# Kernel optimization log

Hardware: AMD Instinct MI355X
Metric: run time of the kernel (lower is better)

Reference implementation:

```python
import jax, jax.numpy as jnp
import numpy as np

N, E, G = 10000, 160000, 64          # nodes, edges, graphs in batch
X_IN, HID, EDIM, H = 128, 128, 32, 4  # feature dims, edge dim, heads
NEG_SLOPE = 0.2


def setup_inputs() -> dict:
    key = jax.random.key(0)
    ks = jax.random.split(key, 24)
    def p(k, shape):
        return jax.random.normal(k, shape, jnp.float32) * 0.1
    inp = {
        "x": jax.random.normal(ks[0], (N, X_IN), jnp.float32),
        "edge_index": jax.random.randint(ks[1], (2, E), 0, N),
        "edge_attr": jax.random.normal(ks[2], (E, EDIM), jnp.float32),
        "batch": jnp.sort(jax.random.randint(ks[3], (N,), 0, G)),
    }
    dims = [(X_IN, HID), (HID, 2 * HID), (2 * HID, HID)]
    i = 4
    for l, (cin, cout) in enumerate(dims, 1):
        inp[f"W{l}"] = p(ks[i], (cin, H * cout)); i += 1   # node lin (bias-free, PyG default)
        inp[f"We{l}"] = p(ks[i], (EDIM, H * cout)); i += 1  # edge lin (bias=False in PyG)
        inp[f"as{l}"] = p(ks[i], (H, cout)); i += 1         # att_src
        inp[f"ad{l}"] = p(ks[i], (H, cout)); i += 1         # att_dst
        inp[f"ae{l}"] = p(ks[i], (H, cout)); i += 1         # att_edge
        inp[f"b{l}"] = jnp.zeros((cout,), jnp.float32); i += 1
    return inp


def _add_self_loops(src, dst, eattr, n):
    # PyG GATConv default: add_self_loops=True, fill_value='mean' ->
    # self-loop edge_attr = scatter-mean of incoming edge_attr per node.
    deg = jax.ops.segment_sum(jnp.ones_like(dst, jnp.float32), dst, num_segments=n)
    mean_e = jax.ops.segment_sum(eattr, dst, num_segments=n) / jnp.maximum(deg, 1.0)[:, None]
    loop = jnp.arange(n)
    return (jnp.concatenate([src, loop]), jnp.concatenate([dst, loop]),
            jnp.concatenate([eattr, mean_e], axis=0))


def _segment_softmax(logits, seg, n):
    # logits: [E2, H], softmax over edges grouped by destination node
    m = jax.ops.segment_max(logits, seg, num_segments=n)
    m = jnp.where(jnp.isfinite(m), m, 0.0)
    ex = jnp.exp(logits - m[seg])
    s = jax.ops.segment_sum(ex, seg, num_segments=n)
    return ex / (s[seg] + 1e-16)


def _gat_layer(x, src, dst, eattr, W, We, a_s, a_d, a_e, b, n):
    heads, cout = a_s.shape
    xs = (x @ W).reshape(n, heads, cout)            # [N,H,C]
    ee = (eattr @ We).reshape(-1, heads, cout)      # [E2,H,C]
    al_src = jnp.sum(xs * a_s, axis=-1)             # [N,H]
    al_dst = jnp.sum(xs * a_d, axis=-1)             # [N,H]
    al_edge = jnp.sum(ee * a_e, axis=-1)            # [E2,H]
    logits = jax.nn.leaky_relu(al_src[src] + al_dst[dst] + al_edge, NEG_SLOPE)
    alpha = _segment_softmax(logits, dst, n)        # [E2,H]
    out = jax.ops.segment_sum(alpha[:, :, None] * xs[src], dst, num_segments=n)
    return out.mean(axis=1) + b                     # concat=False -> mean over heads


def reference(x, edge_index, edge_attr, batch,
              W1, We1, as1, ad1, ae1, b1,
              W2, We2, as2, ad2, ae2, b2,
              W3, We3, as3, ad3, ae3, b3):
    src, dst = edge_index[0], edge_index[1]
    src2, dst2, e2 = _add_self_loops(src, dst, edge_attr, N)
    h = jax.nn.elu(_gat_layer(x, src2, dst2, e2, W1, We1, as1, ad1, ae1, b1, N))
    h = jax.nn.elu(_gat_layer(h, src2, dst2, e2, W2, We2, as2, ad2, ae2, b2, N))
    h = jax.nn.elu(_gat_layer(h, src2, dst2, e2, W3, We3, as3, ad3, ae3, b3, N))
    cnt = jax.ops.segment_sum(jnp.ones((N,), jnp.float32), batch, num_segments=G)
    return jax.ops.segment_sum(h, batch, num_segments=G) / jnp.maximum(cnt, 1.0)[:, None]
```

## Files before the change

kernel.cpp:

```cpp
#include <hip/hip_runtime.h>

#define NN 10000
#define NE 160000
#define NE2 (NE + NN)
#define NG 64
#define EDIM 32

typedef _Float16 f16;
typedef __attribute__((ext_vector_type(2))) _Float16 f16x2;
typedef __attribute__((ext_vector_type(4))) _Float16 f16x4;
typedef __attribute__((ext_vector_type(8))) _Float16 f16x8;
typedef __attribute__((ext_vector_type(4))) float f32x4;
typedef __attribute__((ext_vector_type(8))) unsigned short u16x8;

__device__ __forceinline__ float lrelu(float x) { return fmaxf(x, 0.2f * x); }
__device__ __forceinline__ float elu1(float x) { return x > 0.f ? x : __expf(x) - 1.f; }


__global__ __launch_bounds__(256) void k_prep(const int* __restrict__ ei,
                                              int* __restrict__ deg,
                                              const float* __restrict__ x,
                                              f16* __restrict__ x16) {
    int b = blockIdx.x, tid = threadIdx.x;
    if (b < 625) {
        int e = b * 256 + tid;
        atomicAdd(&deg[ei[NE + e]], 1);
    } else {
        int i = (b - 625) * 256 + tid;
        float4 v = ((const float4*)x)[i];
        f16x4 o;
        o[0] = (f16)v.x; o[1] = (f16)v.y; o[2] = (f16)v.z; o[3] = (f16)v.w;
        *(f16x4*)(x16 + i * 4) = o;
    }
}


__global__ __launch_bounds__(1024) void k_scan2(const int* __restrict__ deg,
                                                int* __restrict__ row_ptr,
                                                int* __restrict__ cursor,
                                                const int* __restrict__ batch,
                                                float* __restrict__ invc) {
    int tid = threadIdx.x;
    int vals[10];
    int run = 0;
#pragma unroll
    for (int i = 0; i < 10; ++i) {
        int n = tid * 10 + i;
        int v = (n < NN) ? (deg[n] + 1) : 0;
        run += v;
        vals[i] = run;
    }
    int total = run;
    int lane = tid & 63, wid = tid >> 6;
    int sc = total;
#pragma unroll
    for (int off = 1; off < 64; off <<= 1) {
        int t = __shfl_up(sc, off);
        if (lane >= off) sc += t;
    }
    __shared__ int wsum[16];
    if (lane == 63) wsum[wid] = sc;
    __syncthreads();
    if (tid == 0) {
        int a = 0;
#pragma unroll
        for (int w = 0; w < 16; ++w) { int t = wsum[w]; wsum[w] = a; a += t; }
    }
    __syncthreads();
    int excl = sc - total + wsum[wid];
#pragma unroll
    for (int i = 0; i < 10; ++i) {
        int n = tid * 10 + i;
        if (n < NN) {
            int prev = i ? vals[i - 1] : 0;
            row_ptr[n + 1] = excl + vals[i];
            cursor[n] = excl + prev;
        }
    }
    if (tid == 0) row_ptr[0] = 0;
    if (tid < NG) {
        int g = tid;
        int lo = 0, hi = NN;
        while (lo < hi) { int mid = (lo + hi) >> 1; if (batch[mid] < g) lo = mid + 1; else hi = mid; }
        int start = lo;
        lo = start; hi = NN;
        while (lo < hi) { int mid = (lo + hi) >> 1; if (batch[mid] < g + 1) lo = mid + 1; else hi = mid; }
        invc[g] = 1.f / fmaxf((float)(lo - start), 1.f);
    }
}

__global__ void k_fill(const int* __restrict__ ei, int* __restrict__ cursor,
                       int* __restrict__ src_sorted, int* __restrict__ eid_sorted,
                       int* __restrict__ pos) {
    int e = blockIdx.x * blockDim.x + threadIdx.x;
    if (e >= NE2) return;
    int s, d;
    if (e < NE) { s = ei[e]; d = ei[NE + e]; }
    else        { s = d = e - NE; }
    int p = atomicAdd(&cursor[d], 1);
    src_sorted[p] = s;
    eid_sorted[p] = e;
    pos[e] = p;
}

__global__ __launch_bounds__(256) void k_esum(const int* __restrict__ row_ptr,
                                              const int* __restrict__ eid_sorted,
                                              const float* __restrict__ eattr,
                                              float* __restrict__ esum) {
    int wid = threadIdx.x >> 6, lane = threadIdx.x & 63;
    int node = blockIdx.x * 4 + wid;
    int d = lane & 31, sel = lane >> 5;
    int beg = row_ptr[node], end = row_ptr[node + 1];
    float v = 0.f;
    for (int j = beg + sel; j < end; j += 2) {
        int eid = eid_sorted[j];
        if (eid < NE) v += eattr[(size_t)eid * EDIM + d];
    }
    v += __shfl_xor(v, 32);
    if (sel == 0) esum[node * EDIM + d] = v;
}


template <int CIN, int C>
__device__ __forceinline__ void wprep_body(int b, int tid,
                                           const float* __restrict__ W,
                                           const float* __restrict__ We,
                                           const float* __restrict__ as_,
                                           const float* __restrict__ ad_,
                                           const float* __restrict__ ae_,
                                           f16* __restrict__ Bt,
                                           float* __restrict__ asd,
                                           float* __restrict__ Wf,
                                           float (*t)[33]) {
    constexpr int K4 = 4 * CIN;
    constexpr int KT = CIN / 32, CT = C / 32;
    constexpr int TB = 4 * KT * CT;
    constexpr int FB = CIN / 64;
    if (b < TB) {
        int h = b / (KT * CT);
        int rem = b % (KT * CT);
        int k0 = (rem / CT) * 32, c0 = (rem % CT) * 32;
        int i = tid >> 5, j = tid & 31;
#pragma unroll
        for (int it = 0; it < 4; ++it)
            t[i + it * 8][j] = W[(size_t)(k0 + i + it * 8) * (4 * C) + h * C + c0 + j];
        __syncthreads();
#pragma unroll
        for (int it = 0; it < 4; ++it) {
            int jj = (tid >> 5) + it * 8, ii = tid & 31;
            Bt[(size_t)(c0 + jj) * K4 + h * CIN + k0 + ii] = (f16)t[ii][jj];
        }
    } else if (b < TB + FB) {
        int k = (b - TB) * 64 + (tid >> 2), h = tid & 3;
        const float4* wr = (const float4*)(W + (size_t)k * (4 * C) + h * C);
        const float4* a4 = (const float4*)(as_ + h * C);
        const float4* d4 = (const float4*)(ad_ + h * C);
        float s = 0.f, d = 0.f;
        for (int c = 0; c < C / 4; ++c) {
            float4 w = wr[c], av = a4[c], dv = d4[c];
            s += w.x * av.x + w.y * av.y + w.z * av.z + w.w * av.w;
            d += w.x * dv.x + w.y * dv.y + w.z * dv.z + w.w * dv.w;
        }
        asd[h * CIN + k] = s;
        asd[4 * CIN + h * CIN + k] = d;
    } else if (tid < 128) {
        int dd = tid >> 2, h = tid & 3;
        const float4* wr = (const float4*)(We + (size_t)dd * (4 * C) + h * C);
        const float4* a4 = (const float4*)(ae_ + h * C);
        float s = 0.f;
        for (int c = 0; c < C / 4; ++c) {
            float4 w = wr[c], av = a4[c];
            s += w.x * av.x + w.y * av.y + w.z * av.z + w.w * av.w;
        }
        Wf[dd * 4 + h] = s;
    }
}

__global__ __launch_bounds__(256) void k_wprep_all(
    const float* W1, const float* We1, const float* as1, const float* ad1, const float* ae1,
    f16* Bt1, float* asd1, float* Wf1,
    const float* W2, const float* We2, const float* as2, const float* ad2, const float* ae2,
    f16* Bt2, float* asd2, float* Wf2,
    const float* W3, const float* We3, const float* as3, const float* ad3, const float* ae3,
    f16* Bt3, float* asd3, float* Wf3) {
    __shared__ float t[32][33];
    int b = blockIdx.x, tid = threadIdx.x;
    if (b < 67)       wprep_body<128, 128>(b,       tid, W1, We1, as1, ad1, ae1, Bt1, asd1, Wf1, t);
    else if (b < 198) wprep_body<128, 256>(b - 67,  tid, W2, We2, as2, ad2, ae2, Bt2, asd2, Wf2, t);
    else              wprep_body<256, 128>(b - 198, tid, W3, We3, as3, ad3, ae3, Bt3, asd3, Wf3, t);
}

__global__ __launch_bounds__(256) void k_e4(const float* __restrict__ eattr,
                                            const float* __restrict__ esum,
                                            const int* __restrict__ deg,
                                            const float* __restrict__ Wf1,
                                            const float* __restrict__ Wf2,
                                            const float* __restrict__ Wf3,
                                            const int* __restrict__ pos,
                                            float* __restrict__ e4all) {
    __shared__ float wf[3][128];
    int tid = threadIdx.x;
    if (tid < 128) { wf[0][tid] = Wf1[tid]; wf[1][tid] = Wf2[tid]; wf[2][tid] = Wf3[tid]; }
    __syncthreads();
    int e = blockIdx.x * 256 + tid;
    if (e >= NE2) return;
    const float4* er;
    float scale = 1.f;
    if (e < NE) {
        er = (const float4*)(eattr + (size_t)e * EDIM);
    } else {
        int n = e - NE;
        er = (const float4*)(esum + (size_t)n * EDIM);
        scale = 1.f / fmaxf((float)deg[n], 1.f);
    }
    float4 v[8];
#pragma unroll
    for (int i = 0; i < 8; ++i) v[i] = er[i];
    int p = pos[e];
#pragma unroll
    for (int l = 0; l < 3; ++l) {
        float a0 = 0.f, a1 = 0.f, a2 = 0.f, a3 = 0.f;
#pragma unroll
        for (int d4 = 0; d4 < 8; ++d4) {
            const float* w = &wf[l][d4 * 16];
            a0 += v[d4].x * w[0] + v[d4].y * w[4] + v[d4].z * w[8]  + v[d4].w * w[12];
            a1 += v[d4].x * w[1] + v[d4].y * w[5] + v[d4].z * w[9]  + v[d4].w * w[13];
            a2 += v[d4].x * w[2] + v[d4].y * w[6] + v[d4].z * w[10] + v[d4].w * w[14];
            a3 += v[d4].x * w[3] + v[d4].y * w[7] + v[d4].z * w[11] + v[d4].w * w[15];
        }
        ((float4*)e4all)[(size_t)l * NE2 + p] =
            make_float4(a0 * scale, a1 * scale, a2 * scale, a3 * scale);
    }
}

template <int CIN>
__global__ __launch_bounds__(256) void k_alnode2(const f16* __restrict__ xp,
                                                 const float* __restrict__ asd,
                                                 float* __restrict__ als,
                                                 float* __restrict__ ald) {
    __shared__ float sA[4 * CIN], sD[4 * CIN];
    for (int i = threadIdx.x; i < 4 * CIN; i += 256) { sA[i] = asd[i]; sD[i] = asd[4 * CIN + i]; }
    __syncthreads();
    int wid = threadIdx.x >> 6, lane = threadIdx.x & 63;
    int node = blockIdx.x * 4 + wid;
    int h = lane >> 4, c16 = lane & 15;
    constexpr int KC = CIN / 16;
    const f16* xr = xp + (size_t)node * CIN + c16 * KC;
    float s = 0.f, d = 0.f;
#pragma unroll
    for (int p = 0; p < KC / 8; ++p) {
        f16x8 v = *(const f16x8*)(xr + p * 8);
        const float* wa = &sA[h * CIN + c16 * KC + p * 8];
        const float* wd = &sD[h * CIN + c16 * KC + p * 8];
#pragma unroll
        for (int i = 0; i < 8; ++i) {
            float f = (float)v[i];
            s += f * wa[i];
            d += f * wd[i];
        }
    }
#pragma unroll
    for (int off = 1; off < 16; off <<= 1) { s += __shfl_xor(s, off); d += __shfl_xor(d, off); }
    if (c16 == 0) { als[node * 4 + h] = s; ald[node * 4 + h] = d; }
}

template <int CIN>
__global__ __launch_bounds__(256) void k_agg2(const int* __restrict__ row_ptr,
                                              const int* __restrict__ src_sorted,
                                              const float* __restrict__ e4,
                                              const float* __restrict__ als,
                                              const float* __restrict__ ald,
                                              const f16* __restrict__ xp,
                                              f16* __restrict__ aggcat) {
    constexpr int EPL = CIN / 64;
    int wid = threadIdx.x >> 6, lane = threadIdx.x & 63;
    int node = blockIdx.x * 4 + wid;
    int beg = row_ptr[node], end = row_ptr[node + 1];
    float4 ad4 = ((const float4*)ald)[node];
    const float4* e44 = (const float4*)e4;
    const float4* als4 = (const float4*)als;
    float s0 = 0.f, s1 = 0.f, s2 = 0.f, s3 = 0.f;
    float a0[EPL] = {}, a1[EPL] = {}, a2[EPL] = {}, a3[EPL] = {};
    const f16* xbase = xp + lane * EPL;
#pragma unroll 4
    for (int j = beg; j < end; ++j) {
        int src = src_sorted[j];
        float4 ev = e44[j];
        float4 av = als4[src];
        float e0 = __expf(lrelu(ev.x + av.x + ad4.x));
        float e1 = __expf(lrelu(ev.y + av.y + ad4.y));
        float e2 = __expf(lrelu(ev.z + av.z + ad4.z));
        float e3 = __expf(lrelu(ev.w + av.w + ad4.w));
        s0 += e0; s1 += e1; s2 += e2; s3 += e3;
        const f16* xr = xbase + (size_t)src * CIN;
        if (EPL == 2) {
            f16x2 v = *(const f16x2*)xr;
            float f0 = (float)v[0], f1 = (float)v[1];
            a0[0] += e0 * f0; a0[1] += e0 * f1;
            a1[0] += e1 * f0; a1[1] += e1 * f1;
            a2[0] += e2 * f0; a2[1] += e2 * f1;
            a3[0] += e3 * f0; a3[1] += e3 * f1;
        } else {
            f16x4 v = *(const f16x4*)xr;
#pragma unroll
            for (int i = 0; i < 4; ++i) {
                float f = (float)v[i];
                a0[i] += e0 * f; a1[i] += e1 * f; a2[i] += e2 * f; a3[i] += e3 * f;
            }
        }
    }
    float i0 = 1.f / (s0 + 1e-16f), i1 = 1.f / (s1 + 1e-16f);
    float i2 = 1.f / (s2 + 1e-16f), i3 = 1.f / (s3 + 1e-16f);
    f16* ob = aggcat + (size_t)node * 4 * CIN + lane * EPL;
    if (EPL == 2) {
        f16x2 o;
        o[0] = (f16)(a0[0] * i0); o[1] = (f16)(a0[1] * i0); *(f16x2*)(ob + 0 * CIN) = o;
        o[0] = (f16)(a1[0] * i1); o[1] = (f16)(a1[1] * i1); *(f16x2*)(ob + 1 * CIN) = o;
        o[0] = (f16)(a2[0] * i2); o[1] = (f16)(a2[1] * i2); *(f16x2*)(ob + 2 * CIN) = o;
        o[0] = (f16)(a3[0] * i3); o[1] = (f16)(a3[1] * i3); *(f16x2*)(ob + 3 * CIN) = o;
    } else {
        f16x4 o;
#pragma unroll
        for (int i = 0; i < 4; ++i) o[i] = (f16)(a0[i] * i0);
        *(f16x4*)(ob + 0 * CIN) = o;
#pragma unroll
        for (int i = 0; i < 4; ++i) o[i] = (f16)(a1[i] * i1);
        *(f16x4*)(ob + 1 * CIN) = o;
#pragma unroll
        for (int i = 0; i < 4; ++i) o[i] = (f16)(a2[i] * i2);
        *(f16x4*)(ob + 2 * CIN) = o;
#pragma unroll
        for (int i = 0; i < 4; ++i) o[i] = (f16)(a3[i] * i3);
        *(f16x4*)(ob + 3 * CIN) = o;
    }
}

template <int K4, int C>
__global__ __launch_bounds__(256) void k_gemm_ep(const f16* __restrict__ A,
                                                 const f16* __restrict__ Bt,
                                                 const float* __restrict__ bias,
                                                 f16* __restrict__ hout) {
    __shared__ f16 Als[64 * 40];
    __shared__ f16 Bls[64 * 40];
    int bm = blockIdx.x * 64, bn = blockIdx.y * 64;
    int tid = threadIdx.x;
    int wid = tid >> 6, lane = tid & 63;
    int wrow = (wid >> 1) * 32, wcol = (wid & 1) * 32;
    int fr = lane & 15, fk = (lane >> 4) * 8;
    f32x4 acc[2][2];
#pragma unroll
    for (int m = 0; m < 2; ++m)
#pragma unroll
        for (int n = 0; n < 2; ++n) acc[m][n] = (f32x4){0.f, 0.f, 0.f, 0.f};

    int srow = tid >> 2, spart = tid & 3;
    for (int k0 = 0; k0 < K4; k0 += 32) {
        int gr = bm + srow;
        u16x8 va = (u16x8)0;
        if (gr < NN) va = *(const u16x8*)(A + (size_t)gr * K4 + k0 + spart * 8);
        *(u16x8*)&Als[srow * 40 + spart * 8] = va;
        u16x8 vb = *(const u16x8*)(Bt + (size_t)(bn + srow) * K4 + k0 + spart * 8);
        *(u16x8*)&Bls[srow * 40 + spart * 8] = vb;
        __syncthreads();
        f16x8 af[2], bf[2];
        af[0] = *(const f16x8*)&Als[(wrow + fr) * 40 + fk];
        af[1] = *(const f16x8*)&Als[(wrow + 16 + fr) * 40 + fk];
        bf[0] = *(const f16x8*)&Bls[(wcol + fr) * 40 + fk];
        bf[1] = *(const f16x8*)&Bls[(wcol + 16 + fr) * 40 + fk];
#pragma unroll
        for (int m = 0; m < 2; ++m)
#pragma unroll
            for (int n = 0; n < 2; ++n)
                acc[m][n] = __builtin_amdgcn_mfma_f32_16x16x32_f16(af[m], bf[n], acc[m][n], 0, 0, 0);
        __syncthreads();
    }

    int cr = (lane >> 4) * 4, cc = lane & 15;
    float b0 = bias[bn + wcol + cc], b1 = bias[bn + wcol + 16 + cc];
#pragma unroll
    for (int m = 0; m < 2; ++m) {
#pragma unroll
        for (int r = 0; r < 4; ++r) {
            int row = bm + wrow + m * 16 + cr + r;
            if (row >= NN) continue;
            f16* cp = hout + (size_t)row * C + bn + wcol + cc;
            cp[0]  = (f16)elu1(0.25f * acc[m][0][r] + b0);
            cp[16] = (f16)elu1(0.25f * acc[m][1][r] + b1);
        }
    }
}

template <int K4, int C>
__global__ __launch_bounds__(256) void k_gemm_pool(const f16* __restrict__ A,
                                                   const f16* __restrict__ Bt,
                                                   const float* __restrict__ bias,
                                                   const int* __restrict__ batch,
                                                   const float* __restrict__ invc,
                                                   float* __restrict__ out) {
    __shared__ f16 Als[64 * 40];
    __shared__ f16 Bls[64 * 40];
    int bm = blockIdx.x * 64, bn = blockIdx.y * 64;
    int tid = threadIdx.x;
    int wid = tid >> 6, lane = tid & 63;
    int wrow = (wid >> 1) * 32, wcol = (wid & 1) * 32;
    int fr = lane & 15, fk = (lane >> 4) * 8;
    f32x4 acc[2][2];
#pragma unroll
    for (int m = 0; m < 2; ++m)
#pragma unroll
        for (int n = 0; n < 2; ++n) acc[m][n] = (f32x4){0.f, 0.f, 0.f, 0.f};

    int srow = tid >> 2, spart = tid & 3;
    for (int k0 = 0; k0 < K4; k0 += 32) {
        int gr = bm + srow;
        u16x8 va = (u16x8)0;
        if (gr < NN) va = *(const u16x8*)(A + (size_t)gr * K4 + k0 + spart * 8);
        *(u16x8*)&Als[srow * 40 + spart * 8] = va;
        u16x8 vb = *(const u16x8*)(Bt + (size_t)(bn + srow) * K4 + k0 + spart * 8);
        *(u16x8*)&Bls[srow * 40 + spart * 8] = vb;
        __syncthreads();
        f16x8 af[2], bf[2];
        af[0] = *(const f16x8*)&Als[(wrow + fr) * 40 + fk];
        af[1] = *(const f16x8*)&Als[(wrow + 16 + fr) * 40 + fk];
        bf[0] = *(const f16x8*)&Bls[(wcol + fr) * 40 + fk];
        bf[1] = *(const f16x8*)&Bls[(wcol + 16 + fr) * 40 + fk];
#pragma unroll
        for (int m = 0; m < 2; ++m)
#pragma unroll
            for (int n = 0; n < 2; ++n)
                acc[m][n] = __builtin_amdgcn_mfma_f32_16x16x32_f16(af[m], bf[n], acc[m][n], 0, 0, 0);
        __syncthreads();
    }

    int cr = (lane >> 4) * 4, cc = lane & 15;
    float b0 = bias[bn + wcol + cc], b1 = bias[bn + wcol + 16 + cc];
#pragma unroll
    for (int m = 0; m < 2; ++m) {
#pragma unroll
        for (int r = 0; r < 4; ++r) {
            int row = bm + wrow + m * 16 + cr + r;
            if (row >= NN) continue;
            int g = batch[row];
            float ic = invc[g];
            float* op = out + (size_t)g * C + bn + wcol + cc;
            atomicAdd(op,      elu1(0.25f * acc[m][0][r] + b0) * ic);
            atomicAdd(op + 16, elu1(0.25f * acc[m][1][r] + b1) * ic);
        }
    }
}


struct Ws {
    f16 *x16, *hA, *hB, *aggcat, *Wt1, *Wt2, *Wt3;
    float *als, *ald, *esum, *e4all, *asd1, *asd2, *asd3, *Wf1, *Wf2, *Wf3, *invc;
    int *deg, *row_ptr, *cursor, *src_sorted, *eid_sorted, *pos;
};

static void carve(void* base, Ws& w) {
    char* p = (char*)base;
    size_t off = 0;
    auto take = [&](size_t bytes) {
        off = (off + 255) & ~(size_t)255;
        void* r = p + off;
        off += bytes;
        return r;
    };
    w.x16        = (f16*)take((size_t)NN * 128 * 2);
    w.hA         = (f16*)take((size_t)NN * 128 * 2);
    w.hB         = (f16*)take((size_t)NN * 256 * 2);
    w.aggcat     = (f16*)take((size_t)NN * 1024 * 2);
    w.Wt1        = (f16*)take((size_t)512 * 128 * 2);
    w.Wt2        = (f16*)take((size_t)512 * 256 * 2);
    w.Wt3        = (f16*)take((size_t)1024 * 128 * 2);
    w.als        = (float*)take((size_t)NN * 4 * 4);
    w.ald        = (float*)take((size_t)NN * 4 * 4);
    w.esum       = (float*)take((size_t)NN * EDIM * 4);
    w.e4all      = (float*)take((size_t)3 * NE2 * 4 * 4);
    w.asd1       = (float*)take(2 * 4 * 128 * 4);
    w.asd2       = (float*)take(2 * 4 * 128 * 4);
    w.asd3       = (float*)take(2 * 4 * 256 * 4);
    w.Wf1        = (float*)take(128 * 4);
    w.Wf2        = (float*)take(128 * 4);
    w.Wf3        = (float*)take(128 * 4);
    w.invc       = (float*)take(NG * 4);
    w.deg        = (int*)take((size_t)NN * 4);
    w.row_ptr    = (int*)take((size_t)(NN + 1) * 4);
    w.cursor     = (int*)take((size_t)NN * 4);
    w.src_sorted = (int*)take((size_t)NE2 * 4);
    w.eid_sorted = (int*)take((size_t)NE2 * 4);
    w.pos        = (int*)take((size_t)NE2 * 4);
}

extern "C" void kernel_launch(void* const* d_in, const int* in_sizes, int n_in,
                              void* d_out, int out_size, void* d_ws, size_t ws_size,
                              hipStream_t stream) {
    const float* x     = (const float*)d_in[0];
    const int*   ei    = (const int*)d_in[1];
    const float* eattr = (const float*)d_in[2];
    const int*   batch = (const int*)d_in[3];
    const float* W[3]  = {(const float*)d_in[4],  (const float*)d_in[10], (const float*)d_in[16]};
    const float* We[3] = {(const float*)d_in[5],  (const float*)d_in[11], (const float*)d_in[17]};
    const float* as_[3]= {(const float*)d_in[6],  (const float*)d_in[12], (const float*)d_in[18]};
    const float* ad_[3]= {(const float*)d_in[7],  (const float*)d_in[13], (const float*)d_in[19]};
    const float* ae_[3]= {(const float*)d_in[8],  (const float*)d_in[14], (const float*)d_in[20]};
    const float* b_[3] = {(const float*)d_in[9],  (const float*)d_in[15], (const float*)d_in[21]};
    float* out = (float*)d_out;

    Ws w;
    carve(d_ws, w);

    hipMemsetAsync(w.deg, 0, (size_t)NN * 4, stream);
    hipMemsetAsync(out, 0, (size_t)NG * 128 * 4, stream);

    k_wprep_all<<<331, 256, 0, stream>>>(
        W[0], We[0], as_[0], ad_[0], ae_[0], w.Wt1, w.asd1, w.Wf1,
        W[1], We[1], as_[1], ad_[1], ae_[1], w.Wt2, w.asd2, w.Wf2,
        W[2], We[2], as_[2], ad_[2], ae_[2], w.Wt3, w.asd3, w.Wf3);

    k_prep<<<1875, 256, 0, stream>>>(ei, w.deg, x, w.x16);
    k_scan2<<<1, 1024, 0, stream>>>(w.deg, w.row_ptr, w.cursor, batch, w.invc);
    k_fill<<<(NE2 + 255) / 256, 256, 0, stream>>>(ei, w.cursor, w.src_sorted,
                                                  w.eid_sorted, w.pos);
    k_esum<<<NN / 4, 256, 0, stream>>>(w.row_ptr, w.eid_sorted, eattr, w.esum);
    k_e4<<<(NE2 + 255) / 256, 256, 0, stream>>>(eattr, w.esum, w.deg,
                                                w.Wf1, w.Wf2, w.Wf3, w.pos, w.e4all);

    const float* e4_1 = w.e4all;
    const float* e4_2 = w.e4all + (size_t)NE2 * 4;
    const float* e4_3 = w.e4all + (size_t)2 * NE2 * 4;

    k_alnode2<128><<<NN / 4, 256, 0, stream>>>(w.x16, w.asd1, w.als, w.ald);
    k_agg2<128><<<NN / 4, 256, 0, stream>>>(w.row_ptr, w.src_sorted, e4_1, w.als, w.ald,
                                            w.x16, w.aggcat);
    k_gemm_ep<512, 128><<<dim3(157, 2), 256, 0, stream>>>(w.aggcat, w.Wt1, b_[0], w.hA);

    k_alnode2<128><<<NN / 4, 256, 0, stream>>>(w.hA, w.asd2, w.als, w.ald);
    k_agg2<128><<<NN / 4, 256, 0, stream>>>(w.row_ptr, w.src_sorted, e4_2, w.als, w.ald,
                                            w.hA, w.aggcat);
    k_gemm_ep<512, 256><<<dim3(157, 4), 256, 0, stream>>>(w.aggcat, w.Wt2, b_[1], w.hB);

    k_alnode2<256><<<NN / 4, 256, 0, stream>>>(w.hB, w.asd3, w.als, w.ald);
    k_agg2<256><<<NN / 4, 256, 0, stream>>>(w.row_ptr, w.src_sorted, e4_3, w.als, w.ald,
                                            w.hB, w.aggcat);
    k_gemm_pool<1024, 128><<<dim3(157, 2), 256, 0, stream>>>(w.aggcat, w.Wt3, b_[2],
                                                             batch, w.invc, out);
}
```

Before: 348.7 us.

## Fuse preprocessing kernels, compute self-loop edge logits from projected values, fold alnode into GEMM epilogue

Merges weight prep, degree counting, x-to-f16 conversion and graph counts into one init kernel, and fuses the CSR fill with edge-logit projection and layer-1 node attention. Self-loop edge logits are now the mean of the already-projected incoming edge logits (linearity), which removes the esum pass, eid_sorted and pos. The layer 2/3 node attention scalars are computed in the previous GEMM epilogue via shuffles and atomics, which removes the separate alnode kernels. The aim is fewer launches and less memory traffic, at the cost of extra atomics and a nondeterministic float summation order.

```diff
diff --git a/kernel.cpp b/kernel.cpp
--- a/kernel.cpp
+++ b/kernel.cpp
@@ -15,110 +15,6 @@
 
 __device__ __forceinline__ float lrelu(float x) { return fmaxf(x, 0.2f * x); }
 __device__ __forceinline__ float elu1(float x) { return x > 0.f ? x : __expf(x) - 1.f; }
-
-
-__global__ __launch_bounds__(256) void k_prep(const int* __restrict__ ei,
-                                              int* __restrict__ deg,
-                                              const float* __restrict__ x,
-                                              f16* __restrict__ x16) {
-    int b = blockIdx.x, tid = threadIdx.x;
-    if (b < 625) {
-        int e = b * 256 + tid;
-        atomicAdd(&deg[ei[NE + e]], 1);
-    } else {
-        int i = (b - 625) * 256 + tid;
-        float4 v = ((const float4*)x)[i];
-        f16x4 o;
-        o[0] = (f16)v.x; o[1] = (f16)v.y; o[2] = (f16)v.z; o[3] = (f16)v.w;
-        *(f16x4*)(x16 + i * 4) = o;
-    }
-}
-
-
-__global__ __launch_bounds__(1024) void k_scan2(const int* __restrict__ deg,
-                                                int* __restrict__ row_ptr,
-                                                int* __restrict__ cursor,
-                                                const int* __restrict__ batch,
-                                                float* __restrict__ invc) {
-    int tid = threadIdx.x;
-    int vals[10];
-    int run = 0;
-#pragma unroll
-    for (int i = 0; i < 10; ++i) {
-        int n = tid * 10 + i;
-        int v = (n < NN) ? (deg[n] + 1) : 0;
-        run += v;
-        vals[i] = run;
-    }
-    int total = run;
-    int lane = tid & 63, wid = tid >> 6;
-    int sc = total;
-#pragma unroll
-    for (int off = 1; off < 64; off <<= 1) {
-        int t = __shfl_up(sc, off);
-        if (lane >= off) sc += t;
-    }
-    __shared__ int wsum[16];
-    if (lane == 63) wsum[wid] = sc;
-    __syncthreads();
-    if (tid == 0) {
-        int a = 0;
-#pragma unroll
-        for (int w = 0; w < 16; ++w) { int t = wsum[w]; wsum[w] = a; a += t; }
-    }
-    __syncthreads();
-    int excl = sc - total + wsum[wid];
-#pragma unroll
-    for (int i = 0; i < 10; ++i) {
-        int n = tid * 10 + i;
-        if (n < NN) {
-            int prev = i ? vals[i - 1] : 0;
-            row_ptr[n + 1] = excl + vals[i];
-            cursor[n] = excl + prev;
-        }
-    }
-    if (tid == 0) row_ptr[0] = 0;
-    if (tid < NG) {
-        int g = tid;
-        int lo = 0, hi = NN;
-        while (lo < hi) { int mid = (lo + hi) >> 1; if (batch[mid] < g) lo = mid + 1; else hi = mid; }
-        int start = lo;
-        lo = start; hi = NN;
-        while (lo < hi) { int mid = (lo + hi) >> 1; if (batch[mid] < g + 1) lo = mid + 1; else hi = mid; }
-        invc[g] = 1.f / fmaxf((float)(lo - start), 1.f);
-    }
-}
-
-__global__ void k_fill(const int* __restrict__ ei, int* __restrict__ cursor,
-                       int* __restrict__ src_sorted, int* __restrict__ eid_sorted,
-                       int* __restrict__ pos) {
-    int e = blockIdx.x * blockDim.x + threadIdx.x;
-    if (e >= NE2) return;
-    int s, d;
-    if (e < NE) { s = ei[e]; d = ei[NE + e]; }
-    else        { s = d = e - NE; }
-    int p = atomicAdd(&cursor[d], 1);
-    src_sorted[p] = s;
-    eid_sorted[p] = e;
-    pos[e] = p;
-}
-
-__global__ __launch_bounds__(256) void k_esum(const int* __restrict__ row_ptr,
-                                              const int* __restrict__ eid_sorted,
-                                              const float* __restrict__ eattr,
-                                              float* __restrict__ esum) {
-    int wid = threadIdx.x >> 6, lane = threadIdx.x & 63;
-    int node = blockIdx.x * 4 + wid;
-    int d = lane & 31, sel = lane >> 5;
-    int beg = row_ptr[node], end = row_ptr[node + 1];
-    float v = 0.f;
-    for (int j = beg + sel; j < end; j += 2) {
-        int eid = eid_sorted[j];
-        if (eid < NE) v += eattr[(size_t)eid * EDIM + d];
-    }
-    v += __shfl_xor(v, 32);
-    if (sel == 0) esum[node * EDIM + d] = v;
-}
 
 
 template <int CIN, int C>
@@ -176,93 +72,178 @@
     }
 }
 
-__global__ __launch_bounds__(256) void k_wprep_all(
+
+__global__ __launch_bounds__(256) void k_init(
     const float* W1, const float* We1, const float* as1, const float* ad1, const float* ae1,
     f16* Bt1, float* asd1, float* Wf1,
     const float* W2, const float* We2, const float* as2, const float* ad2, const float* ae2,
     f16* Bt2, float* asd2, float* Wf2,
     const float* W3, const float* We3, const float* as3, const float* ad3, const float* ae3,
-    f16* Bt3, float* asd3, float* Wf3) {
+    f16* Bt3, float* asd3, float* Wf3,
+    const int* ei, int* deg, const float* x, f16* x16,
+    const int* batch, float* invc) {
     __shared__ float t[32][33];
     int b = blockIdx.x, tid = threadIdx.x;
-    if (b < 67)       wprep_body<128, 128>(b,       tid, W1, We1, as1, ad1, ae1, Bt1, asd1, Wf1, t);
-    else if (b < 198) wprep_body<128, 256>(b - 67,  tid, W2, We2, as2, ad2, ae2, Bt2, asd2, Wf2, t);
-    else              wprep_body<256, 128>(b - 198, tid, W3, We3, as3, ad3, ae3, Bt3, asd3, Wf3, t);
-}
-
-__global__ __launch_bounds__(256) void k_e4(const float* __restrict__ eattr,
-                                            const float* __restrict__ esum,
-                                            const int* __restrict__ deg,
-                                            const float* __restrict__ Wf1,
-                                            const float* __restrict__ Wf2,
-                                            const float* __restrict__ Wf3,
-                                            const int* __restrict__ pos,
-                                            float* __restrict__ e4all) {
-    __shared__ float wf[3][128];
+    if (b < 67) {
+        wprep_body<128, 128>(b, tid, W1, We1, as1, ad1, ae1, Bt1, asd1, Wf1, t);
+    } else if (b < 198) {
+        wprep_body<128, 256>(b - 67, tid, W2, We2, as2, ad2, ae2, Bt2, asd2, Wf2, t);
+    } else if (b < 331) {
+        wprep_body<256, 128>(b - 198, tid, W3, We3, as3, ad3, ae3, Bt3, asd3, Wf3, t);
+    } else if (b < 956) {
+        int e = (b - 331) * 256 + tid;
+        atomicAdd(&deg[ei[NE + e]], 1);
+    } else if (b < 2206) {
+        int i = (b - 956) * 256 + tid;
+        float4 v = ((const float4*)x)[i];
+        f16x4 o;
+        o[0] = (f16)v.x; o[1] = (f16)v.y; o[2] = (f16)v.z; o[3] = (f16)v.w;
+        *(f16x4*)(x16 + i * 4) = o;
+    } else if (tid < NG) {
+        int g = tid;
+        int lo = 0, hi = NN;
+        while (lo < hi) { int mid = (lo + hi) >> 1; if (batch[mid] < g) lo = mid + 1; else hi = mid; }
+        int start = lo;
+        lo = start; hi = NN;
+        while (lo < hi) { int mid = (lo + hi) >> 1; if (batch[mid] < g + 1) lo = mid + 1; else hi = mid; }
+        invc[g] = 1.f / fmaxf((float)(lo - start), 1.f);
+    }
+}
+
+
+__global__ __launch_bounds__(1024) void k_scan2(const int* __restrict__ deg,
+                                                int* __restrict__ row_ptr,
+                                                int* __restrict__ cursor) {
     int tid = threadIdx.x;
-    if (tid < 128) { wf[0][tid] = Wf1[tid]; wf[1][tid] = Wf2[tid]; wf[2][tid] = Wf3[tid]; }
+    int vals[10];
+    int run = 0;
+#pragma unroll
+    for (int i = 0; i < 10; ++i) {
+        int n = tid * 10 + i;
+        int v = (n < NN) ? (deg[n] + 1) : 0;
+        run += v;
+        vals[i] = run;
+    }
+    int total = run;
+    int lane = tid & 63, wid = tid >> 6;
+    int sc = total;
+#pragma unroll
+    for (int off = 1; off < 64; off <<= 1) {
+        int t = __shfl_up(sc, off);
+        if (lane >= off) sc += t;
+    }
+    __shared__ int wsum[16];
+    if (lane == 63) wsum[wid] = sc;
     __syncthreads();
-    int e = blockIdx.x * 256 + tid;
-    if (e >= NE2) return;
-    const float4* er;
-    float scale = 1.f;
-    if (e < NE) {
-        er = (const float4*)(eattr + (size_t)e * EDIM);
+    if (tid == 0) {
+        int a = 0;
+#pragma unroll
+        for (int w = 0; w < 16; ++w) { int t = wsum[w]; wsum[w] = a; a += t; }
+    }
+    __syncthreads();
+    int excl = sc - total + wsum[wid];
+#pragma unroll
+    for (int i = 0; i < 10; ++i) {
+        int n = tid * 10 + i;
+        if (n < NN) {
+            int prev = i ? vals[i - 1] : 0;
+            row_ptr[n + 1] = excl + vals[i];
+            cursor[n] = excl + prev;
+        }
+    }
+    if (tid == 0) row_ptr[0] = 0;
+}
+
+
+__global__ __launch_bounds__(256) void k_fill_e4(const int* __restrict__ ei,
+                                                 int* __restrict__ cursor,
+                                                 int* __restrict__ src_sorted,
+                                                 int* __restrict__ selfpos,
+                                                 const float* __restrict__ eattr,
+                                                 const float* __restrict__ Wf1,
+                                                 const float* __restrict__ Wf2,
+                                                 const float* __restrict__ Wf3,
+                                                 float* __restrict__ e4all,
+                                                 const f16* __restrict__ x16,
+                                                 const float* __restrict__ asd1,
+                                                 float* __restrict__ als1,
+                                                 float* __restrict__ ald1) {
+    __shared__ float smem[1024];
+    int b = blockIdx.x, tid = threadIdx.x;
+    if (b < 665) {
+        for (int i = tid; i < 384; i += 256)
+            smem[i] = (i < 128) ? Wf1[i] : (i < 256) ? Wf2[i - 128] : Wf3[i - 256];
+        __syncthreads();
+        int e = b * 256 + tid;
+        if (e >= NE2) return;
+        if (e < NE) {
+            int s = ei[e], d = ei[NE + e];
+            int p = atomicAdd(&cursor[d], 1);
+            src_sorted[p] = s;
+            float4 v[8];
+            const float4* er = (const float4*)(eattr + (size_t)e * EDIM);
+#pragma unroll
+            for (int i = 0; i < 8; ++i) v[i] = er[i];
+#pragma unroll
+            for (int l = 0; l < 3; ++l) {
+                float a0 = 0.f, a1 = 0.f, a2 = 0.f, a3 = 0.f;
+#pragma unroll
+                for (int d4 = 0; d4 < 8; ++d4) {
+                    const float* w = &smem[l * 128 + d4 * 16];
+                    a0 += v[d4].x * w[0] + v[d4].y * w[4] + v[d4].z * w[8]  + v[d4].w * w[12];
+                    a1 += v[d4].x * w[1] + v[d4].y * w[5] + v[d4].z * w[9]  + v[d4].w * w[13];
+                    a2 += v[d4].x * w[2] + v[d4].y * w[6] + v[d4].z * w[10] + v[d4].w * w[14];
+                    a3 += v[d4].x * w[3] + v[d4].y * w[7] + v[d4].z * w[11] + v[d4].w * w[15];
+                }
+                ((float4*)e4all)[(size_t)l * NE2 + p] = make_float4(a0, a1, a2, a3);
+            }
+        } else {
+            int n = e - NE;
+            int p = atomicAdd(&cursor[n], 1);
+            src_sorted[p] = n;
+            selfpos[n] = p;
+        }
     } else {
-        int n = e - NE;
-        er = (const float4*)(esum + (size_t)n * EDIM);
-        scale = 1.f / fmaxf((float)deg[n], 1.f);
-    }
-    float4 v[8];
-#pragma unroll
-    for (int i = 0; i < 8; ++i) v[i] = er[i];
-    int p = pos[e];
-#pragma unroll
-    for (int l = 0; l < 3; ++l) {
-        float a0 = 0.f, a1 = 0.f, a2 = 0.f, a3 = 0.f;
-#pragma unroll
-        for (int d4 = 0; d4 < 8; ++d4) {
-            const float* w = &wf[l][d4 * 16];
-            a0 += v[d4].x * w[0] + v[d4].y * w[4] + v[d4].z * w[8]  + v[d4].w * w[12];
-            a1 += v[d4].x * w[1] + v[d4].y * w[5] + v[d4].z * w[9]  + v[d4].w * w[13];
-            a2 += v[d4].x * w[2] + v[d4].y * w[6] + v[d4].z * w[10] + v[d4].w * w[14];
-            a3 += v[d4].x * w[3] + v[d4].y * w[7] + v[d4].z * w[11] + v[d4].w * w[15];
-        }
-        ((float4*)e4all)[(size_t)l * NE2 + p] =
-            make_float4(a0 * scale, a1 * scale, a2 * scale, a3 * scale);
-    }
-}
-
-template <int CIN>
-__global__ __launch_bounds__(256) void k_alnode2(const f16* __restrict__ xp,
-                                                 const float* __restrict__ asd,
-                                                 float* __restrict__ als,
-                                                 float* __restrict__ ald) {
-    __shared__ float sA[4 * CIN], sD[4 * CIN];
-    for (int i = threadIdx.x; i < 4 * CIN; i += 256) { sA[i] = asd[i]; sD[i] = asd[4 * CIN + i]; }
-    __syncthreads();
-    int wid = threadIdx.x >> 6, lane = threadIdx.x & 63;
-    int node = blockIdx.x * 4 + wid;
-    int h = lane >> 4, c16 = lane & 15;
-    constexpr int KC = CIN / 16;
-    const f16* xr = xp + (size_t)node * CIN + c16 * KC;
-    float s = 0.f, d = 0.f;
-#pragma unroll
-    for (int p = 0; p < KC / 8; ++p) {
-        f16x8 v = *(const f16x8*)(xr + p * 8);
-        const float* wa = &sA[h * CIN + c16 * KC + p * 8];
-        const float* wd = &sD[h * CIN + c16 * KC + p * 8];
+        float* sA = smem;
+        float* sD = smem + 512;
+        for (int i = tid; i < 512; i += 256) { sA[i] = asd1[i]; sD[i] = asd1[512 + i]; }
+        __syncthreads();
+        int wid = tid >> 6, lane = tid & 63;
+        int node = (b - 665) * 4 + wid;
+        int h = lane >> 4, c16 = lane & 15;
+        const f16* xr = x16 + (size_t)node * 128 + c16 * 8;
+        f16x8 v = *(const f16x8*)xr;
+        float s = 0.f, d = 0.f;
 #pragma unroll
         for (int i = 0; i < 8; ++i) {
             float f = (float)v[i];
-            s += f * wa[i];
-            d += f * wd[i];
-        }
-    }
-#pragma unroll
-    for (int off = 1; off < 16; off <<= 1) { s += __shfl_xor(s, off); d += __shfl_xor(d, off); }
-    if (c16 == 0) { als[node * 4 + h] = s; ald[node * 4 + h] = d; }
-}
+            s += f * sA[h * 128 + c16 * 8 + i];
+            d += f * sD[h * 128 + c16 * 8 + i];
+        }
+#pragma unroll
+        for (int off = 1; off < 16; off <<= 1) { s += __shfl_xor(s, off); d += __shfl_xor(d, off); }
+        if (c16 == 0) { als1[node * 4 + h] = s; ald1[node * 4 + h] = d; }
+    }
+}
+
+
+__global__ __launch_bounds__(256) void k_e4self(const int* __restrict__ row_ptr,
+                                                const int* __restrict__ selfpos,
+                                                float* __restrict__ e4all) {
+    int t = blockIdx.x * 256 + threadIdx.x;
+    int node = t >> 4, sub = t & 15;
+    if (sub >= 12) return;
+    int l = sub >> 2, c = sub & 3;
+    int beg = row_ptr[node], end = row_ptr[node + 1];
+    int sp = selfpos[node];
+    const float* base = e4all + (size_t)l * NE2 * 4 + c;
+    float s = 0.f;
+    for (int j = beg; j < end; ++j)
+        if (j != sp) s += base[(size_t)j * 4];
+    float inv = 1.f / fmaxf((float)(end - beg - 1), 1.f);
+    e4all[(size_t)l * NE2 * 4 + (size_t)sp * 4 + c] = s * inv;
+}
+
 
 template <int CIN>
 __global__ __launch_bounds__(256) void k_agg2(const int* __restrict__ row_ptr,
@@ -335,11 +316,15 @@
     }
 }
 
-template <int K4, int C>
+
+template <int K4, int C, bool FUSE>
 __global__ __launch_bounds__(256) void k_gemm_ep(const f16* __restrict__ A,
                                                  const f16* __restrict__ Bt,
                                                  const float* __restrict__ bias,
-                                                 f16* __restrict__ hout) {
+                                                 f16* __restrict__ hout,
+                                                 const float* __restrict__ asd_n,
+                                                 float* __restrict__ als_n,
+                                                 float* __restrict__ ald_n) {
     __shared__ f16 Als[64 * 40];
     __shared__ f16 Bls[64 * 40];
     int bm = blockIdx.x * 64, bn = blockIdx.y * 64;
@@ -376,19 +361,56 @@
     }
 
     int cr = (lane >> 4) * 4, cc = lane & 15;
-    float b0 = bias[bn + wcol + cc], b1 = bias[bn + wcol + 16 + cc];
+    int col0 = bn + wcol + cc, col1 = col0 + 16;
+    float b0 = bias[col0], b1 = bias[col1];
+    float wa0[4], wa1[4], wd0[4], wd1[4];
+    if (FUSE) {
+#pragma unroll
+        for (int h = 0; h < 4; ++h) {
+            wa0[h] = asd_n[h * C + col0];
+            wa1[h] = asd_n[h * C + col1];
+            wd0[h] = asd_n[4 * C + h * C + col0];
+            wd1[h] = asd_n[4 * C + h * C + col1];
+        }
+    }
 #pragma unroll
     for (int m = 0; m < 2; ++m) {
 #pragma unroll
         for (int r = 0; r < 4; ++r) {
             int row = bm + wrow + m * 16 + cr + r;
             if (row >= NN) continue;
-            f16* cp = hout + (size_t)row * C + bn + wcol + cc;
-            cp[0]  = (f16)elu1(0.25f * acc[m][0][r] + b0);
-            cp[16] = (f16)elu1(0.25f * acc[m][1][r] + b1);
-        }
-    }
-}
+            float v0 = elu1(0.25f * acc[m][0][r] + b0);
+            float v1 = elu1(0.25f * acc[m][1][r] + b1);
+            f16* cp = hout + (size_t)row * C + col0;
+            cp[0]  = (f16)v0;
+            cp[16] = (f16)v1;
+            if (FUSE) {
+                float s[4], d[4];
+#pragma unroll
+                for (int h = 0; h < 4; ++h) {
+                    s[h] = v0 * wa0[h] + v1 * wa1[h];
+                    d[h] = v0 * wd0[h] + v1 * wd1[h];
+                }
+#pragma unroll
+                for (int off = 1; off < 16; off <<= 1) {
+#pragma unroll
+                    for (int h = 0; h < 4; ++h) {
+                        s[h] += __shfl_xor(s[h], off);
+                        d[h] += __shfl_xor(d[h], off);
+                    }
+                }
+                if (cc == 0) {
+#pragma unroll
+                    for (int h = 0; h < 4; ++h) {
+                        atomicAdd(&als_n[row * 4 + h], s[h]);
+                        atomicAdd(&ald_n[row * 4 + h], d[h]);
+                    }
+                }
+            }
+        }
+    }
+}
+
 
 template <int K4, int C>
 __global__ __launch_bounds__(256) void k_gemm_pool(const f16* __restrict__ A,
@@ -452,8 +474,11 @@
 
 struct Ws {
     f16 *x16, *hA, *hB, *aggcat, *Wt1, *Wt2, *Wt3;
-    float *als, *ald, *esum, *e4all, *asd1, *asd2, *asd3, *Wf1, *Wf2, *Wf3, *invc;
-    int *deg, *row_ptr, *cursor, *src_sorted, *eid_sorted, *pos;
+    float *als1, *ald1;
+    int *deg;
+    float *als2, *ald2, *als3, *ald3;
+    float *e4all, *asd1, *asd2, *asd3, *Wf1, *Wf2, *Wf3, *invc;
+    int *row_ptr, *cursor, *src_sorted, *selfpos;
 };
 
 static void carve(void* base, Ws& w) {
@@ -472,9 +497,13 @@
     w.Wt1        = (f16*)take((size_t)512 * 128 * 2);
     w.Wt2        = (f16*)take((size_t)512 * 256 * 2);
     w.Wt3        = (f16*)take((size_t)1024 * 128 * 2);
-    w.als        = (float*)take((size_t)NN * 4 * 4);
-    w.ald        = (float*)take((size_t)NN * 4 * 4);
-    w.esum       = (float*)take((size_t)NN * EDIM * 4);
+    w.als1       = (float*)take((size_t)NN * 4 * 4);
+    w.ald1       = (float*)take((size_t)NN * 4 * 4);
+    w.deg        = (int*)take((size_t)NN * 4);
+    w.als2       = (float*)take((size_t)NN * 4 * 4);
+    w.ald2       = (float*)take((size_t)NN * 4 * 4);
+    w.als3       = (float*)take((size_t)NN * 4 * 4);
+    w.ald3       = (float*)take((size_t)NN * 4 * 4);
     w.e4all      = (float*)take((size_t)3 * NE2 * 4 * 4);
     w.asd1       = (float*)take(2 * 4 * 128 * 4);
     w.asd2       = (float*)take(2 * 4 * 128 * 4);
@@ -483,12 +512,10 @@
     w.Wf2        = (float*)take(128 * 4);
     w.Wf3        = (float*)take(128 * 4);
     w.invc       = (float*)take(NG * 4);
-    w.deg        = (int*)take((size_t)NN * 4);
     w.row_ptr    = (int*)take((size_t)(NN + 1) * 4);
     w.cursor     = (int*)take((size_t)NN * 4);
     w.src_sorted = (int*)take((size_t)NE2 * 4);
-    w.eid_sorted = (int*)take((size_t)NE2 * 4);
-    w.pos        = (int*)take((size_t)NE2 * 4);
+    w.selfpos    = (int*)take((size_t)NN * 4);
 }
 
 extern "C" void kernel_launch(void* const* d_in, const int* in_sizes, int n_in,
@@ -509,38 +536,36 @@
     Ws w;
     carve(d_ws, w);
 
-    hipMemsetAsync(w.deg, 0, (size_t)NN * 4, stream);
+    size_t zspan = (size_t)((char*)w.ald3 - (char*)w.deg) + (size_t)NN * 4 * 4;
+    hipMemsetAsync(w.deg, 0, zspan, stream);
     hipMemsetAsync(out, 0, (size_t)NG * 128 * 4, stream);
 
-    k_wprep_all<<<331, 256, 0, stream>>>(
+    k_init<<<2207, 256, 0, stream>>>(
         W[0], We[0], as_[0], ad_[0], ae_[0], w.Wt1, w.asd1, w.Wf1,
         W[1], We[1], as_[1], ad_[1], ae_[1], w.Wt2, w.asd2, w.Wf2,
-        W[2], We[2], as_[2], ad_[2], ae_[2], w.Wt3, w.asd3, w.Wf3);
-
-    k_prep<<<1875, 256, 0, stream>>>(ei, w.deg, x, w.x16);
-    k_scan2<<<1, 1024, 0, stream>>>(w.deg, w.row_ptr, w.cursor, batch, w.invc);
-    k_fill<<<(NE2 + 255) / 256, 256, 0, stream>>>(ei, w.cursor, w.src_sorted,
-                                                  w.eid_sorted, w.pos);
-    k_esum<<<NN / 4, 256, 0, stream>>>(w.row_ptr, w.eid_sorted, eattr, w.esum);
-    k_e4<<<(NE2 + 255) / 256, 256, 0, stream>>>(eattr, w.esum, w.deg,
-                                                w.Wf1, w.Wf2, w.Wf3, w.pos, w.e4all);
+        W[2], We[2], as_[2], ad_[2], ae_[2], w.Wt3, w.asd3, w.Wf3,
+        ei, w.deg, x, w.x16, batch, w.invc);
+
+    k_scan2<<<1, 1024, 0, stream>>>(w.deg, w.row_ptr, w.cursor);
+
+    k_fill_e4<<<3165, 256, 0, stream>>>(ei, w.cursor, w.src_sorted, w.selfpos, eattr,
+                                        w.Wf1, w.Wf2, w.Wf3, w.e4all,
+                                        w.x16, w.asd1, w.als1, w.ald1);
+    k_e4self<<<625, 256, 0, stream>>>(w.row_ptr, w.selfpos, w.e4all);
 
     const float* e4_1 = w.e4all;
     const float* e4_2 = w.e4all + (size_t)NE2 * 4;
     const float* e4_3 = w.e4all + (size_t)2 * NE2 * 4;
 
-    k_alnode2<128><<<NN / 4, 256, 0, stream>>>(w.x16, w.asd1, w.als, w.ald);
-    k_agg2<128><<<NN / 4, 256, 0, stream>>>(w.row_ptr, w.src_sorted, e4_1, w.als, w.ald,
+    k_agg2<128><<<NN / 4, 256, 0, stream>>>(w.row_ptr, w.src_sorted, e4_1, w.als1, w.ald1,
                                             w.x16, w.aggcat);
-    k_gemm_ep<512, 128><<<dim3(157, 2), 256, 0, stream>>>(w.aggcat, w.Wt1, b_[0], w.hA);
-
-    k_alnode2<128><<<NN / 4, 256, 0, stream>>>(w.hA, w.asd2, w.als, w.ald);
-    k_agg2<128><<<NN / 4, 256, 0, stream>>>(w.row_ptr, w.src_sorted, e4_2, w.als, w.ald,
+    k_gemm_ep<512, 128, true><<<dim3(157, 2), 256, 0, stream>>>(w.aggcat, w.Wt1, b_[0],
+                                                                w.hA, w.asd2, w.als2, w.ald2);
+    k_agg2<128><<<NN / 4, 256, 0, stream>>>(w.row_ptr, w.src_sorted, e4_2, w.als2, w.ald2,
                                             w.hA, w.aggcat);
-    k_gemm_ep<512, 256><<<dim3(157, 4), 256, 0, stream>>>(w.aggcat, w.Wt2, b_[1], w.hB);
-
-    k_alnode2<256><<<NN / 4, 256, 0, stream>>>(w.hB, w.asd3, w.als, w.ald);
-    k_agg2<256><<<NN / 4, 256, 0, stream>>>(w.row_ptr, w.src_sorted, e4_3, w.als, w.ald,
+    k_gemm_ep<512, 256, true><<<dim3(157, 4), 256, 0, stream>>>(w.aggcat, w.Wt2, b_[1],
+                                                                w.hB, w.asd3, w.als3, w.ald3);
+    k_agg2<256><<<NN / 4, 256, 0, stream>>>(w.row_ptr, w.src_sorted, e4_3, w.als3, w.ald3,
                                             w.hB, w.aggcat);
     k_gemm_pool<1024, 128><<<dim3(157, 2), 256, 0, stream>>>(w.aggcat, w.Wt3, b_[2],
                                                              batch, w.invc, out);
```

Measured after the change: 363.6 us. 1.04x slower.
